# Optimization experiments

Measured on AMD Instinct MI355X. Metric: run time of the kernel, lower is better.

## Reference

```python
import jax, jax.numpy as jnp
import numpy as np

N, E, H, K = 50000, 300000, 128, 50
PI = float(np.pi)
EPS = 1e-5


def gaussian_expand(ea, k):
    # RBF expansion of each edge feature into k gaussians on [0, 1]
    centers = jnp.linspace(0.0, 1.0, k)            # (k,)
    width = 1.0 / k
    g = jnp.exp(-((ea[..., None] - centers) ** 2) / (2.0 * width * width))  # (E, 4, k)
    return g.reshape(ea.shape[0], -1)              # (E, 4k)


def bn_train(z, g, b):
    # BatchNorm1d in training mode: biased batch stats
    m = jnp.mean(z, axis=0)
    v = jnp.mean(z * z, axis=0) - m * m
    return (z - m) * jax.lax.rsqrt(v + EPS) * g + b


def lrelu(z):
    return jnp.where(z >= 0, z, 0.01 * z)


def setup_inputs() -> dict:
    key = jax.random.key(0)
    ks = jax.random.split(key, 16)
    s = 0.02
    d = {
        "x": jax.random.normal(ks[0], (N, H), jnp.float32),
        "edge_attr": jax.random.uniform(ks[1], (E, 4), jnp.float32),
        "edge_index": jax.random.randint(ks[2], (2, E), 0, N, jnp.int32),
        # f_b: Linear(4K -> H)
        "Wb": jax.random.normal(ks[3], (4 * K, H), jnp.float32) * s,
        "bb": jnp.zeros((H,), jnp.float32),
        # f_e: Linear(3H->H) + LReLU + BN + Linear(H->H) + LReLU + BN + Linear(H->H)
        "We1": jax.random.normal(ks[4], (3 * H, H), jnp.float32) * s,
        "be1": jnp.zeros((H,), jnp.float32),
        "ge1": jnp.ones((H,), jnp.float32),
        "bte1": jnp.zeros((H,), jnp.float32),
        "We2": jax.random.normal(ks[5], (H, H), jnp.float32) * s,
        "be2": jnp.zeros((H,), jnp.float32),
        "ge2": jnp.ones((H,), jnp.float32),
        "bte2": jnp.zeros((H,), jnp.float32),
        "We3": jax.random.normal(ks[6], (H, H), jnp.float32) * s,
        "be3": jnp.zeros((H,), jnp.float32),
        # f_d: Linear(H->H)
        "Wd": jax.random.normal(ks[7], (H, H), jnp.float32) * s,
        "bd": jnp.zeros((H,), jnp.float32),
        # v parameter (1, H)
        "v": jnp.ones((1, H), jnp.float32),
        # f_n: Linear(H->H) + LReLU + BN + Linear(H->H)
        "Wn1": jax.random.normal(ks[8], (H, H), jnp.float32) * s,
        "bn1": jnp.zeros((H,), jnp.float32),
        "gn": jnp.ones((H,), jnp.float32),
        "btn": jnp.zeros((H,), jnp.float32),
        "Wn2": jax.random.normal(ks[9], (H, H), jnp.float32) * s,
        "bn2": jnp.zeros((H,), jnp.float32),
    }
    return d


def reference(x, edge_attr, edge_index, Wb, bb, We1, be1, ge1, bte1, We2, be2,
              ge2, bte2, We3, be3, Wd, bd, v, Wn1, bn1, gn, btn, Wn2, bn2):
    src, dst = edge_index[0], edge_index[1]
    gt = gaussian_expand(edge_attr, K) @ Wb + bb            # (E, H)
    coeff = jnp.cos(PI / 2 * edge_attr[:, 3])[:, None]      # (E, 1)
    h = jnp.concatenate([x[src], gt, x[dst]], axis=1)       # (E, 3H)
    h = bn_train(lrelu(h @ We1 + be1), ge1, bte1)
    h = bn_train(lrelu(h @ We2 + be2), ge2, bte2)
    cond_filter = coeff * (h @ We3 + be3)                   # (E, H)
    m_st = cond_filter * (x[src] @ Wd + bd)                 # (E, H)
    m_t = v * (x @ Wd + bd)                                 # (N, H)
    incoming = jax.ops.segment_sum(m_st, dst, num_segments=N)  # scatter_add + zero pad
    z = m_t + incoming
    out = bn_train(lrelu(z @ Wn1 + bn1), gn, btn) @ Wn2 + bn2 + x
    return out
```

## Files before the change

kernel.cpp:

```cpp
#include <hip/hip_runtime.h>

typedef __attribute__((ext_vector_type(8))) short bf16x8;
typedef __attribute__((ext_vector_type(4))) float f32x4;
typedef __attribute__((ext_vector_type(4))) unsigned uint32x4;

#define DEVFN __device__ __forceinline__

DEVFN short f2bf(float f) {
    union { float f; unsigned u; } v; v.f = f;
    unsigned r = (v.u + 0x7FFFu + ((v.u >> 16) & 1u)) >> 16;
    return (short)(unsigned short)r;
}
DEVFN float bf2f(short h) {
    union { unsigned u; float f; } v; v.u = ((unsigned)(unsigned short)h) << 16;
    return v.f;
}
DEVFN unsigned pkbf(float a, float b) {
    unsigned r;
    asm("v_cvt_pk_bf16_f32 %0, %1, %2" : "=v"(r) : "v"(a), "v"(b));
    return r;
}

#define GLD_LDS16(gp, lp)                                                     \
    __builtin_amdgcn_global_load_lds(                                         \
        (const __attribute__((address_space(1))) unsigned*)(gp),              \
        (__attribute__((address_space(3))) unsigned*)(lp), 16, 0, 0)

struct __align__(16) ERec { int src; int dst; float cf; int pad; float4 ea; };



__global__ __launch_bounds__(128) void build_w1p_k(
    const float* __restrict__ Wb, const float* __restrict__ We1,
    const float* __restrict__ bb, const float* __restrict__ be1,
    float* __restrict__ W1p, float* __restrict__ b1p)
{
    int j = threadIdx.x;
    const float* B = We1 + 128 * 128;
    int i = blockIdx.x;
    if (i < 200) {
        float a = 0.f;
        for (int m = 0; m < 128; m++) a += Wb[i * 128 + m] * B[m * 128 + j];
        W1p[i * 128 + j] = a;
    } else {
        float a = be1[j];
        for (int m = 0; m < 128; m++) a += bb[m] * B[m * 128 + j];
        b1p[j] = a;
    }
}

__global__ __launch_bounds__(128) void build_tab_k(
    const float* __restrict__ W1p, const float* __restrict__ b1p,
    unsigned* __restrict__ tabP)
{
    int i = blockIdx.x;
    int c = blockIdx.y;
    int j = threadIdx.x;
    float t0 = (float)i * (1.0f / 1024.0f);
    float t1 = (float)(i + 1) * (1.0f / 1024.0f);
    float base = (c == 0) ? b1p[j] : 0.f;
    float a0 = base, a1 = base;
    int kc = (int)(t0 * 49.f + 0.5f);
    for (int dk = -6; dk <= 7; dk++) {
        int k = kc + dk;
        if (k >= 0 && k < 50) {
            float w = W1p[(c * 50 + k) * 128 + j];
            float d0 = t0 - (float)k * (1.f / 49.f);
            float d1 = t1 - (float)k * (1.f / 49.f);
            a0 += expf(-1250.f * d0 * d0) * w;
            a1 += expf(-1250.f * d1 * d1) * w;
        }
    }
    float v0 = bf2f(f2bf(a0));
    float v1 = bf2f(f2bf(a1));
    unsigned lo = (unsigned)(unsigned short)f2bf(a0);
    unsigned hi = (unsigned)(unsigned short)f2bf(v1 - v0);
    tabP[((size_t)(c * 1024 + i)) * 128 + j] = lo | (hi << 16);
}

__global__ __launch_bounds__(256) void fold_plain_k(
    const float* __restrict__ W0, const float* __restrict__ W1,
    const float* __restrict__ W2, const float* __restrict__ W3,
    short* __restrict__ O0, short* __restrict__ O1,
    short* __restrict__ O2, short* __restrict__ O3)
{
    const float* W = (blockIdx.y == 0) ? W0 : (blockIdx.y == 1) ? W1 : (blockIdx.y == 2) ? W2 : W3;
    short* O = (blockIdx.y == 0) ? O0 : (blockIdx.y == 1) ? O1 : (blockIdx.y == 2) ? O2 : O3;
    int idx = blockIdx.x * 256 + threadIdx.x;
    int n = idx >> 8, ks = (idx >> 6) & 3, lane = idx & 63;
    int k8 = ks * 32 + (lane >> 4) * 8;
    int pcol = (lane & 15) * 8 + n;
    bf16x8 fv;
    #pragma unroll
    for (int i2 = 0; i2 < 8; i2++) fv[i2] = f2bf(W[(k8 + i2) * 128 + pcol]);
    *(bf16x8*)(O + (size_t)idx * 8) = fv;
}

__global__ __launch_bounds__(256) void fold_k(
    const float* __restrict__ W, const float* __restrict__ bias,
    const float* __restrict__ statsG, const float* __restrict__ gamma,
    const float* __restrict__ beta, float invNs,
    short* __restrict__ Bp, float* __restrict__ biasOut)
{
    __shared__ float sS[128], sT[128];
    int tid = threadIdx.x;
    if (tid < 128) {
        float sum = 0.f, sq = 0.f;
        for (int r = 0; r < 16; r++) {
            sum += statsG[r * 256 + tid];
            sq  += statsG[r * 256 + 128 + tid];
        }
        float m = sum * invNs;
        float var = sq * invNs - m * m;
        float rs = rsqrtf(var + 1e-5f);
        float s = rs * gamma[tid];
        float t = beta[tid] - m * s;
        sS[tid] = s; sT[tid] = t;
    }
    __syncthreads();
    if (blockIdx.x == 0 && tid < 128) {
        float b = bias[tid];
        for (int k = 0; k < 128; k++) b += sT[k] * W[k * 128 + tid];
        biasOut[tid] = b;
    }
    int idx = blockIdx.x * 256 + tid;
    int n = idx >> 8, ks = (idx >> 6) & 3, lane = idx & 63;
    int k8 = ks * 32 + (lane >> 4) * 8;
    int pcol = (lane & 15) * 8 + n;
    bf16x8 fv;
    #pragma unroll
    for (int i2 = 0; i2 < 8; i2++)
        fv[i2] = f2bf(sS[k8 + i2] * W[(k8 + i2) * 128 + pcol]);
    *(bf16x8*)(Bp + (size_t)idx * 8) = fv;
}


__global__ __launch_bounds__(256) void hist_k(
    const int* __restrict__ dstI, int* __restrict__ cnt, int E)
{
    int e = blockIdx.x * 256 + threadIdx.x;
    if (e < E) atomicAdd(&cnt[dstI[e]], 1);
}

__global__ __launch_bounds__(256) void scan1_k(
    const int* __restrict__ cnt, int Nn, int* __restrict__ posE, int* __restrict__ bsum)
{
    __shared__ int s[256];
    int t = threadIdx.x, g = blockIdx.x * 256 + t;
    int v = (g < Nn) ? cnt[g] : 0;
    s[t] = v;
    __syncthreads();
    for (int off = 1; off < 256; off <<= 1) {
        int u = (t >= off) ? s[t - off] : 0;
        __syncthreads();
        s[t] += u;
        __syncthreads();
    }
    if (g < Nn) posE[g] = s[t] - v;
    if (t == 255) bsum[blockIdx.x] = s[255];
}

__global__ __launch_bounds__(256) void scan2_k(int* __restrict__ bsum, int nb)
{
    __shared__ int s[256];
    int t = threadIdx.x;
    int v = (t < nb) ? bsum[t] : 0;
    s[t] = v;
    __syncthreads();
    for (int off = 1; off < 256; off <<= 1) {
        int u = (t >= off) ? s[t - off] : 0;
        __syncthreads();
        s[t] += u;
        __syncthreads();
    }
    if (t < nb) bsum[t] = s[t] - v;
}

__global__ __launch_bounds__(256) void fix_k(
    const int* __restrict__ posE, const int* __restrict__ bsum,
    int* __restrict__ pos2, int Nn)
{
    int id = blockIdx.x * 256 + threadIdx.x;
    if (id < Nn) pos2[id] = posE[id] + bsum[id >> 8];
}

__global__ __launch_bounds__(256) void scat_k(
    const int* __restrict__ srcI, const int* __restrict__ dstI,
    const float4* __restrict__ ea4, int* __restrict__ pos2,
    ERec* __restrict__ rec, int E)
{
    int e = blockIdx.x * 256 + threadIdx.x;
    if (e >= E) return;
    int d = dstI[e];
    int p = atomicAdd(&pos2[d], 1);
    float4 ev = ea4[e];
    ERec r;
    r.src = srcI[e]; r.dst = d;
    r.cf = cosf(1.57079632679f * ev.w); r.pad = 0;
    r.ea = ev;
    rec[p] = r;
}

__global__ __launch_bounds__(256, 4) void node_all_k(
    const float* __restrict__ x, int M,
    const short* __restrict__ bp3,
    const float* __restrict__ bd, const float* __restrict__ vv,
    short* __restrict__ xd, short* __restrict__ zaccb,
    short* __restrict__ xs1b, short* __restrict__ xt1b)
{
    int tid = threadIdx.x;
    int wave = tid >> 6, lane = tid & 63;
    int kgrp = lane >> 4, colbase = lane & 15;
    int chunk = blockIdx.x;
    int rowA = chunk * 64 + wave * 16 + colbase;
    bool rv = rowA < M;

    bf16x8 af[4];
    #pragma unroll
    for (int ks = 0; ks < 4; ks++) {
        bf16x8 v = (bf16x8){0,0,0,0,0,0,0,0};
        if (rv) {
            const float* ap = x + (size_t)rowA * 128 + ks * 32 + kgrp * 8;
            float4 f0 = ((const float4*)ap)[0];
            float4 f1 = ((const float4*)ap)[1];
            v[0] = f2bf(f0.x); v[1] = f2bf(f0.y); v[2] = f2bf(f0.z); v[3] = f2bf(f0.w);
            v[4] = f2bf(f1.x); v[5] = f2bf(f1.y); v[6] = f2bf(f1.z); v[7] = f2bf(f1.w);
        }
        af[ks] = v;
    }

    float bcol[8], vcol[8];
    *(float4*)&bcol[0] = *(const float4*)(bd + colbase * 8);
    *(float4*)&bcol[4] = *(const float4*)(bd + colbase * 8 + 4);
    *(float4*)&vcol[0] = *(const float4*)(vv + colbase * 8);
    *(float4*)&vcol[4] = *(const float4*)(vv + colbase * 8 + 4);

    int rbase = chunk * 64 + wave * 16 + kgrp * 4;

    for (int b = 0; b < 3; b++) {
        const short* Bb = bp3 + (size_t)b * 16384;
        f32x4 acc[8];
        #pragma unroll
        for (int n = 0; n < 8; n++) acc[n] = (f32x4){0.f, 0.f, 0.f, 0.f};
        #pragma unroll
        for (int ks = 0; ks < 4; ks++) {
            #pragma unroll
            for (int n = 0; n < 8; n++) {
                bf16x8 bf = *(const bf16x8*)(Bb + ((size_t)((n * 4 + ks) * 64 + lane)) * 8);
                acc[n] = __builtin_amdgcn_mfma_f32_16x16x32_bf16(af[ks], bf, acc[n], 0, 0, 0);
            }
        }
        if (b == 0) {
            #pragma unroll
            for (int r = 0; r < 4; r++) {
                int row = rbase + r;
                if (row < M) {
                    bf16x8 xo, zo;
                    #pragma unroll
                    for (int n = 0; n < 8; n++) {
                        float val = acc[n][r] + bcol[n];
                        xo[n] = f2bf(val);
                        zo[n] = f2bf(vcol[n] * val);
                    }
                    *(bf16x8*)(xd    + (size_t)row * 128 + colbase * 8) = xo;
                    *(bf16x8*)(zaccb + (size_t)row * 128 + colbase * 8) = zo;
                }
            }
        } else {
            short* outp = (b == 1) ? xs1b : xt1b;
            #pragma unroll
            for (int r = 0; r < 4; r++) {
                int row = rbase + r;
                if (row < M) {
                    bf16x8 o;
                    #pragma unroll
                    for (int n = 0; n < 8; n++) o[n] = f2bf(acc[n][r]);
                    *(bf16x8*)(outp + (size_t)row * 128 + colbase * 8) = o;
                }
            }
        }
    }
}


#define EZ_ISSUE(XS, XT, TA, TB, FV, qi) do {                                  \
    int e_ = (qi) * 4 + esub;                                                  \
    int ec_ = e_ < Etot ? e_ : Etot - 1;                                       \
    const ERec* rp_ = rec + ec_;                                               \
    int4 h_ = *(const int4*)rp_;                                               \
    float4 ea_ = *(const float4*)((const char*)rp_ + 16);                      \
    int s_ = h_.x;                                                             \
    int d_ = h_.y;                                                             \
    XS = *(const bf16x8*)(xs1b + (size_t)s_ * 128 + colg * 8);                 \
    XT = *(const bf16x8*)(xt1b + (size_t)d_ * 128 + colg * 8);                 \
    float tv_[4] = {ea_.x, ea_.y, ea_.z, ea_.w};                               \
    _Pragma("unroll")                                                          \
    for (int c_ = 0; c_ < 4; c_++) {                                           \
        float u_ = tv_[c_] * 1024.f;                                           \
        int i0_ = (int)u_;                                                     \
        i0_ = i0_ < 0 ? 0 : (i0_ > 1023 ? 1023 : i0_);                         \
        FV[c_] = u_ - (float)i0_;                                              \
        const uint32x4* tp_ = (const uint32x4*)(tabP +                         \
            ((size_t)(c_ * 1024 + i0_) * 128) + colg * 8);                     \
        TA[c_] = tp_[0];                                                       \
        TB[c_] = tp_[1];                                                       \
    }                                                                          \
} while (0)

#define EZ_CONSUME(XS, XT, TA, TB, FV, qi) do {                                \
    int e_ = (qi) * 4 + esub;                                                  \
    float p_[8];                                                               \
    _Pragma("unroll")                                                          \
    for (int j_ = 0; j_ < 8; j_++) p_[j_] = bf2f(XS[j_]) + bf2f(XT[j_]);       \
    _Pragma("unroll")                                                          \
    for (int c_ = 0; c_ < 4; c_++) {                                           \
        float f_ = FV[c_];                                                     \
        _Pragma("unroll")                                                      \
        for (int j_ = 0; j_ < 4; j_++) {                                       \
            unsigned ua_ = TA[c_][j_];                                         \
            p_[j_] = fmaf(f_, __uint_as_float(ua_ & 0xffff0000u),              \
                          p_[j_] + __uint_as_float(ua_ << 16));                \
            unsigned ub_ = TB[c_][j_];                                         \
            p_[j_ + 4] = fmaf(f_, __uint_as_float(ub_ & 0xffff0000u),          \
                              p_[j_ + 4] + __uint_as_float(ub_ << 16));        \
        }                                                                      \
    }                                                                          \
    bool valid_ = e_ < Etot;                                                   \
    _Pragma("unroll")                                                          \
    for (int j_ = 0; j_ < 8; j_++) {                                           \
        float z_ = p_[j_] >= 0.f ? p_[j_] : 0.01f * p_[j_];                    \
        p_[j_] = z_;                                                           \
        float m_ = valid_ ? z_ : 0.f;                                          \
        sacc[j_] += m_;                                                        \
        qacc[j_] = fmaf(m_, z_, qacc[j_]);                                     \
    }                                                                          \
    if (valid_) {                                                              \
        uint32x4 ov_ = {pkbf(p_[0], p_[1]), pkbf(p_[2], p_[3]),                \
                        pkbf(p_[4], p_[5]), pkbf(p_[6], p_[7])};               \
        *(uint32x4*)(z1 + (size_t)e_ * 128 + colg * 8) = ov_;                  \
    }                                                                          \
} while (0)

__global__ __launch_bounds__(256) void edge_z1_k(
    const short* __restrict__ xs1b, const short* __restrict__ xt1b,
    const unsigned* __restrict__ tabP,
    const ERec* __restrict__ rec,
    short* __restrict__ z1, float* __restrict__ stats, int Etot)
{
    int tid = threadIdx.x, wave = tid >> 6, lane = tid & 63;
    int colg = lane & 15, esub = lane >> 4;

    int gw = blockIdx.x * 4 + wave;
    int W = gridDim.x * 4;
    int nq = (Etot + 3) >> 2;
    int q0 = (int)(((long long)gw * nq) / W);
    int q1 = (int)(((long long)(gw + 1) * nq) / W);
    int nsteps = q1 - q0;

    float sacc[8], qacc[8];
    #pragma unroll
    for (int j = 0; j < 8; j++) { sacc[j] = 0.f; qacc[j] = 0.f; }

    bf16x8 xsA, xtA; uint32x4 taA[4], tbA[4]; float fvA[4];
    bf16x8 xsB, xtB; uint32x4 taB[4], tbB[4]; float fvB[4];
    bf16x8 xsC, xtC; uint32x4 taC[4], tbC[4]; float fvC[4];

    if (nsteps > 0) {
        EZ_ISSUE(xsA, xtA, taA, tbA, fvA, q0 + 0);
        EZ_ISSUE(xsB, xtB, taB, tbB, fvB, q0 + 1);
        int st = 0;
        for (; st + 3 <= nsteps; st += 3) {
            EZ_ISSUE(xsC, xtC, taC, tbC, fvC, q0 + st + 2);
            EZ_CONSUME(xsA, xtA, taA, tbA, fvA, q0 + st);
            EZ_ISSUE(xsA, xtA, taA, tbA, fvA, q0 + st + 3);
            EZ_CONSUME(xsB, xtB, taB, tbB, fvB, q0 + st + 1);
            EZ_ISSUE(xsB, xtB, taB, tbB, fvB, q0 + st + 4);
            EZ_CONSUME(xsC, xtC, taC, tbC, fvC, q0 + st + 2);
        }
        if (st < nsteps)
            EZ_CONSUME(xsA, xtA, taA, tbA, fvA, q0 + st);
        if (st + 1 < nsteps)
            EZ_CONSUME(xsB, xtB, taB, tbB, fvB, q0 + st + 1);
    }

    #pragma unroll
    for (int j = 0; j < 8; j++) {
        sacc[j] += __shfl_xor(sacc[j], 16);
        sacc[j] += __shfl_xor(sacc[j], 32);
        qacc[j] += __shfl_xor(qacc[j], 16);
        qacc[j] += __shfl_xor(qacc[j], 32);
    }

    __shared__ float lS[128], lQ[128];
    if (tid < 128) { lS[tid] = 0.f; lQ[tid] = 0.f; }
    __syncthreads();
    if (esub == 0) {
        #pragma unroll
        for (int j = 0; j < 8; j++) {
            atomicAdd(&lS[colg * 8 + j], sacc[j]);
            atomicAdd(&lQ[colg * 8 + j], qacc[j]);
        }
    }
    __syncthreads();
    if (tid < 128) {
        int rep = blockIdx.x & 15;
        atomicAdd(&stats[rep * 256 + tid], lS[tid]);
        atomicAdd(&stats[rep * 256 + 128 + tid], lQ[tid]);
    }
}

__global__ __launch_bounds__(256) void segred_k(
    const short* __restrict__ cond, const short* __restrict__ xd,
    const ERec* __restrict__ rec, const int* __restrict__ endPos,
    short* __restrict__ zaccb, int Nn)
{
    int tid = threadIdx.x, wave = tid >> 6, lane = tid & 63;
    int colg = lane & 7;
    int esub = lane >> 3;
    int d0 = blockIdx.x * 32 + wave * 8;

    for (int i = 0; i < 8; i++) {
        int d = d0 + i;
        if (d >= Nn) break;
        int s0 = (d == 0) ? 0 : endPos[d - 1];
        int s1 = endPos[d];
        if (s1 <= s0) continue;

        float acc[16];
        #pragma unroll
        for (int j = 0; j < 16; j++) acc[j] = 0.f;

        for (int t = s0 + esub; t < s1; t += 8) {
            const short* cp = cond + (size_t)t * 128 + colg * 16;
            bf16x8 c0 = *(const bf16x8*)cp;
            bf16x8 c1 = *(const bf16x8*)(cp + 8);
            int s = rec[t].src;
            const short* xp = xd + (size_t)s * 128 + colg * 16;
            bf16x8 x0 = *(const bf16x8*)xp;
            bf16x8 x1 = *(const bf16x8*)(xp + 8);
            #pragma unroll
            for (int j = 0; j < 8; j++) {
                acc[j]     += bf2f(c0[j]) * bf2f(x0[j]);
                acc[8 + j] += bf2f(c1[j]) * bf2f(x1[j]);
            }
        }

        #pragma unroll
        for (int j = 0; j < 16; j++) {
            acc[j] += __shfl_xor(acc[j], 8);
            acc[j] += __shfl_xor(acc[j], 16);
            acc[j] += __shfl_xor(acc[j], 32);
        }

        if (esub == 0) {
            short* zp = zaccb + (size_t)d * 128 + colg * 16;
            bf16x8 z0 = *(const bf16x8*)zp;
            bf16x8 z1 = *(const bf16x8*)(zp + 8);
            bf16x8 o0, o1;
            #pragma unroll
            for (int j = 0; j < 8; j++) {
                o0[j] = f2bf(bf2f(z0[j]) + acc[j]);
                o1[j] = f2bf(bf2f(z1[j]) + acc[8 + j]);
            }
            *(bf16x8*)zp = o0;
            *(bf16x8*)(zp + 8) = o1;
        }
    }
}

template<int EPI>
__global__ __launch_bounds__(256, 2) void pgemm_k(
    const short* __restrict__ A, int M,
    const short* __restrict__ Bp, const float* __restrict__ bias,
    void* __restrict__ out, float* __restrict__ stats,
    const ERec* __restrict__ rec, const float* __restrict__ xres)
{
    __shared__ __align__(16) short ldsB[16384];
    __shared__ float lS[128], lQ[128];
    int tid = threadIdx.x;
    int wave = tid >> 6, lane = tid & 63;
    int kgrp = lane >> 4, colbase = lane & 15;

    #pragma unroll
    for (int i = 0; i < 8; i++) {
        int off = (i * 256 + wave * 64 + lane) * 8;
        GLD_LDS16(Bp + off, ldsB + off);
    }

    int nch = (M + 63) >> 6;
    int cbeg = (int)(((long long)blockIdx.x * nch) / gridDim.x);
    int cend = (int)(((long long)(blockIdx.x + 1) * nch) / gridDim.x);

    bf16x8 afc[4];
    {
        int rowA = cbeg * 64 + wave * 16 + colbase;
        bool rv = (cbeg < cend) && (rowA < M);
        #pragma unroll
        for (int ks = 0; ks < 4; ks++)
            afc[ks] = rv ? *(const bf16x8*)(A + (size_t)rowA * 128 + ks * 32 + kgrp * 8)
                         : (bf16x8){0,0,0,0,0,0,0,0};
    }

    float bcol[8];
    *(float4*)&bcol[0] = *(const float4*)(bias + colbase * 8);
    *(float4*)&bcol[4] = *(const float4*)(bias + colbase * 8 + 4);

    float sreg[8], qreg[8];
    if (EPI == 2) {
        #pragma unroll
        for (int n = 0; n < 8; n++) { sreg[n] = 0.f; qreg[n] = 0.f; }
        if (tid < 128) { lS[tid] = 0.f; lQ[tid] = 0.f; }
    }

    __syncthreads();

    for (int c = cbeg; c < cend; c++) {
        int cn = c + 1;
        bf16x8 afn[4];
        {
            int rowA = cn * 64 + wave * 16 + colbase;
            bool rv = (cn < cend) && (rowA < M);
            #pragma unroll
            for (int ks = 0; ks < 4; ks++)
                afn[ks] = rv ? *(const bf16x8*)(A + (size_t)rowA * 128 + ks * 32 + kgrp * 8)
                             : (bf16x8){0,0,0,0,0,0,0,0};
        }

        int rbase = c * 64 + wave * 16 + kgrp * 4;

        float mcf[4];
        if (EPI == 3) {
            #pragma unroll
            for (int r = 0; r < 4; r++) {
                int row = rbase + r;
                mcf[r] = (row < M) ? rec[row].cf : 0.f;
            }
        }

        f32x4 acc[8];
        #pragma unroll
        for (int n = 0; n < 8; n++) acc[n] = (f32x4){0.f, 0.f, 0.f, 0.f};
        #pragma unroll
        for (int ks = 0; ks < 4; ks++) {
            #pragma unroll
            for (int n = 0; n < 8; n++) {
                bf16x8 bf = *(const bf16x8*)(ldsB + ((size_t)((n * 4 + ks) * 64 + lane)) * 8);
                acc[n] = __builtin_amdgcn_mfma_f32_16x16x32_bf16(afc[ks], bf, acc[n], 0, 0, 0);
            }
        }

        if (EPI == 2) {
            short* outh = (short*)out;
            #pragma unroll
            for (int r = 0; r < 4; r++) {
                int row = rbase + r;
                float zz[8];
                #pragma unroll
                for (int n = 0; n < 8; n++) {
                    float z = acc[n][r] + bcol[n];
                    z = z >= 0.f ? z : 0.01f * z;
                    if (row >= M) z = 0.f;
                    sreg[n] += z; qreg[n] += z * z;
                    zz[n] = z;
                }
                if (row < M) {
                    uint32x4 ov = {pkbf(zz[0], zz[1]), pkbf(zz[2], zz[3]),
                                   pkbf(zz[4], zz[5]), pkbf(zz[6], zz[7])};
                    *(uint32x4*)(outh + (size_t)row * 128 + colbase * 8) = ov;
                }
            }
        } else if (EPI == 3) {
            short* outh = (short*)out;
            #pragma unroll
            for (int r = 0; r < 4; r++) {
                int row = rbase + r;
                if (row < M) {
                    float zz[8];
                    #pragma unroll
                    for (int n = 0; n < 8; n++)
                        zz[n] = mcf[r] * (acc[n][r] + bcol[n]);
                    uint32x4 ov = {pkbf(zz[0], zz[1]), pkbf(zz[2], zz[3]),
                                   pkbf(zz[4], zz[5]), pkbf(zz[6], zz[7])};
                    *(uint32x4*)(outh + (size_t)row * 128 + colbase * 8) = ov;
                }
            }
        } else if (EPI == 4) {
            float* outf = (float*)out;
            #pragma unroll
            for (int r = 0; r < 4; r++) {
                int row = rbase + r;
                if (row < M) {
                    const float4* xr = (const float4*)(xres + (size_t)row * 128 + colbase * 8);
                    float4 x0 = xr[0], x1 = xr[1];
                    float4 o0, o1;
                    o0.x = acc[0][r] + bcol[0] + x0.x;
                    o0.y = acc[1][r] + bcol[1] + x0.y;
                    o0.z = acc[2][r] + bcol[2] + x0.z;
                    o0.w = acc[3][r] + bcol[3] + x0.w;
                    o1.x = acc[4][r] + bcol[4] + x1.x;
                    o1.y = acc[5][r] + bcol[5] + x1.y;
                    o1.z = acc[6][r] + bcol[6] + x1.z;
                    o1.w = acc[7][r] + bcol[7] + x1.w;
                    float4* op = (float4*)(outf + (size_t)row * 128 + colbase * 8);
                    op[0] = o0; op[1] = o1;
                }
            }
        }

        #pragma unroll
        for (int ks = 0; ks < 4; ks++) afc[ks] = afn[ks];
    }

    if (EPI == 2) {
        __syncthreads();
        #pragma unroll
        for (int n = 0; n < 8; n++) {
            atomicAdd(&lS[colbase * 8 + n], sreg[n]);
            atomicAdd(&lQ[colbase * 8 + n], qreg[n]);
        }
        __syncthreads();
        if (tid < 128) {
            int rep = blockIdx.x & 15;
            atomicAdd(&stats[rep * 256 + tid], lS[tid]);
            atomicAdd(&stats[rep * 256 + 128 + tid], lQ[tid]);
        }
    }
}

extern "C" void kernel_launch(void* const* d_in, const int* in_sizes, int n_in,
                              void* d_out, int out_size, void* d_ws, size_t ws_size,
                              hipStream_t stream)
{
    const float* x    = (const float*)d_in[0];
    const float* ea   = (const float*)d_in[1];
    const int*   eidx = (const int*)d_in[2];
    const float* Wb   = (const float*)d_in[3];
    const float* bb   = (const float*)d_in[4];
    const float* We1  = (const float*)d_in[5];
    const float* be1  = (const float*)d_in[6];
    const float* ge1  = (const float*)d_in[7];
    const float* bte1 = (const float*)d_in[8];
    const float* We2  = (const float*)d_in[9];
    const float* be2  = (const float*)d_in[10];
    const float* ge2  = (const float*)d_in[11];
    const float* bte2 = (const float*)d_in[12];
    const float* We3  = (const float*)d_in[13];
    const float* be3  = (const float*)d_in[14];
    const float* Wd   = (const float*)d_in[15];
    const float* bd   = (const float*)d_in[16];
    const float* vv   = (const float*)d_in[17];
    const float* Wn1  = (const float*)d_in[18];
    const float* bn1  = (const float*)d_in[19];
    const float* gn   = (const float*)d_in[20];
    const float* btn  = (const float*)d_in[21];
    const float* Wn2  = (const float*)d_in[22];
    const float* bn2  = (const float*)d_in[23];

    const int NN = in_sizes[0] / 128;
    const int EE = in_sizes[1] / 4;

    char* ws = (char*)d_ws;
    size_t oEZ   = 0;
    size_t oXD   = oEZ   + (size_t)EE * 256;
    size_t oXS   = oXD   + (size_t)NN * 256;
    size_t oXT   = oXS   + (size_t)NN * 256;
    size_t oZACC = oXT   + (size_t)NN * 256;
    size_t oZN   = oZACC + (size_t)NN * 256;
    size_t oTAB  = oZN   + (size_t)NN * 256;
    size_t oW1P  = oTAB  + (size_t)4 * 1024 * 512;
    size_t oB1P  = oW1P  + (size_t)200 * 512;
    size_t oBP   = oB1P  + 512;
    size_t oBIAS = oBP   + (size_t)7 * 32768;
    size_t oST   = oBIAS + (size_t)7 * 512;
    size_t oCNT  = oST   + 49152;
    size_t oPOS  = oCNT  + 201728;
    size_t oBSUM = oPOS  + 201728;
    size_t oPOS2 = oBSUM + 1024;
    size_t oREC  = (oPOS2 + 201728 + 31) & ~(size_t)31;

    short* eZ    = (short*)(ws + oEZ);
    short* xd    = (short*)(ws + oXD);
    short* xs1b  = (short*)(ws + oXS);
    short* xt1b  = (short*)(ws + oXT);
    short* zaccb = (short*)(ws + oZACC);
    short* zn    = (short*)(ws + oZN);
    unsigned* tabP = (unsigned*)(ws + oTAB);
    float* W1p   = (float*)(ws + oW1P);
    float* b1p   = (float*)(ws + oB1P);
    short* bp    = (short*)(ws + oBP);
    short* BpW2  = bp + 3 * 16384;
    short* BpW3  = bp + 4 * 16384;
    short* BpN1  = bp + 5 * 16384;
    short* BpN2  = bp + 6 * 16384;
    float* bo    = (float*)(ws + oBIAS);
    float* b2p   = bo + 0 * 128;
    float* b3p   = bo + 1 * 128;
    float* b2np  = bo + 2 * 128;
    float* st1   = (float*)(ws + oST);
    float* st2   = st1 + 4096;
    float* stN   = st1 + 8192;
    int*   cnt   = (int*)(ws + oCNT);
    int*   posE  = (int*)(ws + oPOS);
    int*   bsum  = (int*)(ws + oBSUM);
    int*   pos2  = (int*)(ws + oPOS2);
    ERec*  rec   = (ERec*)(ws + oREC);

    hipMemsetAsync(ws + oST, 0, 49152 + 201728, stream);

    build_w1p_k<<<201, 128, 0, stream>>>(Wb, We1, bb, be1, W1p, b1p);
    build_tab_k<<<dim3(1024, 4), 128, 0, stream>>>(W1p, b1p, tabP);
    fold_plain_k<<<dim3(8, 4), 256, 0, stream>>>(
        Wd, We1, We1 + 256 * 128, Wn1, bp, bp + 16384, bp + 2 * 16384, BpN1);

    int nchN = (NN + 63) / 64;
    int nchE = (EE + 63) / 64;
    int nbN = (NN + 255) / 256;
    int nbE = (EE + 255) / 256;
    int nbSeg = (NN + 31) / 32;

    int gridEz = 1024;
    int gridE = nchE < 1024 ? nchE : 1024;
    int gridN = nchN < 512 ? nchN : 512;

    node_all_k<<<nchN, 256, 0, stream>>>(x, NN, bp, bd, vv, xd, zaccb, xs1b, xt1b);

    hist_k<<<nbE, 256, 0, stream>>>(eidx + EE, cnt, EE);
    scan1_k<<<nbN, 256, 0, stream>>>(cnt, NN, posE, bsum);
    scan2_k<<<1, 256, 0, stream>>>(bsum, nbN);
    fix_k<<<nbN, 256, 0, stream>>>(posE, bsum, pos2, NN);
    scat_k<<<nbE, 256, 0, stream>>>(eidx, eidx + EE, (const float4*)ea, pos2,
                                    rec, EE);

    edge_z1_k<<<gridEz, 256, 0, stream>>>(xs1b, xt1b, tabP, rec, eZ, st1, EE);

    fold_k<<<8, 256, 0, stream>>>(We2, be2, st1, ge1, bte1, 1.f / (float)EE, BpW2, b2p);
    pgemm_k<2><<<gridE, 256, 0, stream>>>(eZ, EE, BpW2, b2p, eZ, st2,
        nullptr, nullptr);

    fold_k<<<8, 256, 0, stream>>>(We3, be3, st2, ge2, bte2, 1.f / (float)EE, BpW3, b3p);
    pgemm_k<3><<<gridE, 256, 0, stream>>>(eZ, EE, BpW3, b3p, eZ, nullptr,
        rec, nullptr);

    segred_k<<<nbSeg, 256, 0, stream>>>(eZ, xd, rec, pos2, zaccb, NN);

    pgemm_k<2><<<gridN, 256, 0, stream>>>(zaccb, NN, BpN1, bn1, zn, stN,
        nullptr, nullptr);

    fold_k<<<8, 256, 0, stream>>>(Wn2, bn2, stN, gn, btn, 1.f / (float)NN, BpN2, b2np);
    pgemm_k<4><<<gridN, 256, 0, stream>>>(zn, NN, BpN2, b2np, d_out, nullptr,
        nullptr, x);
}
```

Baseline: 400.8 us.

## Use finer nearest-neighbor bf16 Gaussian table and deepen A-fragment prefetch in pgemm

```diff
diff --git a/kernel.cpp b/kernel.cpp
--- a/kernel.cpp
+++ b/kernel.cpp
@@ -51,31 +51,23 @@
 
 __global__ __launch_bounds__(128) void build_tab_k(
     const float* __restrict__ W1p, const float* __restrict__ b1p,
-    unsigned* __restrict__ tabP)
+    short* __restrict__ tabN)
 {
     int i = blockIdx.x;
     int c = blockIdx.y;
     int j = threadIdx.x;
-    float t0 = (float)i * (1.0f / 1024.0f);
-    float t1 = (float)(i + 1) * (1.0f / 1024.0f);
-    float base = (c == 0) ? b1p[j] : 0.f;
-    float a0 = base, a1 = base;
-    int kc = (int)(t0 * 49.f + 0.5f);
-    for (int dk = -6; dk <= 7; dk++) {
+    float t = ((float)i + 0.5f) * (1.0f / 4096.0f);
+    float acc = (c == 0) ? b1p[j] : 0.f;
+    int kc = (int)(t * 49.f + 0.5f);
+    for (int dk = -6; dk <= 6; dk++) {
         int k = kc + dk;
         if (k >= 0 && k < 50) {
-            float w = W1p[(c * 50 + k) * 128 + j];
-            float d0 = t0 - (float)k * (1.f / 49.f);
-            float d1 = t1 - (float)k * (1.f / 49.f);
-            a0 += expf(-1250.f * d0 * d0) * w;
-            a1 += expf(-1250.f * d1 * d1) * w;
-        }
-    }
-    float v0 = bf2f(f2bf(a0));
-    float v1 = bf2f(f2bf(a1));
-    unsigned lo = (unsigned)(unsigned short)f2bf(a0);
-    unsigned hi = (unsigned)(unsigned short)f2bf(v1 - v0);
-    tabP[((size_t)(c * 1024 + i)) * 128 + j] = lo | (hi << 16);
+            float d = t - (float)k * (1.f / 49.f);
+            float g = expf(-1250.f * d * d);
+            acc += g * W1p[(c * 50 + k) * 128 + j];
+        }
+    }
+    tabN[((size_t)(c * 4096 + i)) * 128 + j] = f2bf(acc);
 }
 
 __global__ __launch_bounds__(256) void fold_plain_k(
@@ -283,47 +275,33 @@
 }
 
 
-#define EZ_ISSUE(XS, XT, TA, TB, FV, qi) do {                                  \
+#define EZ_ISSUE(XS, XT, TT, qi) do {                                          \
     int e_ = (qi) * 4 + esub;                                                  \
     int ec_ = e_ < Etot ? e_ : Etot - 1;                                       \
     const ERec* rp_ = rec + ec_;                                               \
     int4 h_ = *(const int4*)rp_;                                               \
     float4 ea_ = *(const float4*)((const char*)rp_ + 16);                      \
-    int s_ = h_.x;                                                             \
-    int d_ = h_.y;                                                             \
-    XS = *(const bf16x8*)(xs1b + (size_t)s_ * 128 + colg * 8);                 \
-    XT = *(const bf16x8*)(xt1b + (size_t)d_ * 128 + colg * 8);                 \
+    XS = *(const bf16x8*)(xs1b + (size_t)h_.x * 128 + colg * 8);               \
+    XT = *(const bf16x8*)(xt1b + (size_t)h_.y * 128 + colg * 8);               \
     float tv_[4] = {ea_.x, ea_.y, ea_.z, ea_.w};                               \
     _Pragma("unroll")                                                          \
     for (int c_ = 0; c_ < 4; c_++) {                                           \
-        float u_ = tv_[c_] * 1024.f;                                           \
-        int i0_ = (int)u_;                                                     \
-        i0_ = i0_ < 0 ? 0 : (i0_ > 1023 ? 1023 : i0_);                         \
-        FV[c_] = u_ - (float)i0_;                                              \
-        const uint32x4* tp_ = (const uint32x4*)(tabP +                         \
-            ((size_t)(c_ * 1024 + i0_) * 128) + colg * 8);                     \
-        TA[c_] = tp_[0];                                                       \
-        TB[c_] = tp_[1];                                                       \
+        int i0_ = (int)(tv_[c_] * 4096.f);                                     \
+        i0_ = i0_ < 0 ? 0 : (i0_ > 4095 ? 4095 : i0_);                         \
+        TT[c_] = *(const bf16x8*)(tabN +                                       \
+            ((size_t)(c_ * 4096 + i0_) * 128) + colg * 8);                     \
     }                                                                          \
 } while (0)
 
-#define EZ_CONSUME(XS, XT, TA, TB, FV, qi) do {                                \
+#define EZ_CONSUME(XS, XT, TT, qi) do {                                        \
     int e_ = (qi) * 4 + esub;                                                  \
     float p_[8];                                                               \
     _Pragma("unroll")                                                          \
     for (int j_ = 0; j_ < 8; j_++) p_[j_] = bf2f(XS[j_]) + bf2f(XT[j_]);       \
     _Pragma("unroll")                                                          \
     for (int c_ = 0; c_ < 4; c_++) {                                           \
-        float f_ = FV[c_];                                                     \
         _Pragma("unroll")                                                      \
-        for (int j_ = 0; j_ < 4; j_++) {                                       \
-            unsigned ua_ = TA[c_][j_];                                         \
-            p_[j_] = fmaf(f_, __uint_as_float(ua_ & 0xffff0000u),              \
-                          p_[j_] + __uint_as_float(ua_ << 16));                \
-            unsigned ub_ = TB[c_][j_];                                         \
-            p_[j_ + 4] = fmaf(f_, __uint_as_float(ub_ & 0xffff0000u),          \
-                              p_[j_ + 4] + __uint_as_float(ub_ << 16));        \
-        }                                                                      \
+        for (int j_ = 0; j_ < 8; j_++) p_[j_] += bf2f(TT[c_][j_]);             \
     }                                                                          \
     bool valid_ = e_ < Etot;                                                   \
     _Pragma("unroll")                                                          \
@@ -343,7 +321,7 @@
 
 __global__ __launch_bounds__(256) void edge_z1_k(
     const short* __restrict__ xs1b, const short* __restrict__ xt1b,
-    const unsigned* __restrict__ tabP,
+    const short* __restrict__ tabN,
     const ERec* __restrict__ rec,
     short* __restrict__ z1, float* __restrict__ stats, int Etot)
 {
@@ -361,26 +339,26 @@
     #pragma unroll
     for (int j = 0; j < 8; j++) { sacc[j] = 0.f; qacc[j] = 0.f; }
 
-    bf16x8 xsA, xtA; uint32x4 taA[4], tbA[4]; float fvA[4];
-    bf16x8 xsB, xtB; uint32x4 taB[4], tbB[4]; float fvB[4];
-    bf16x8 xsC, xtC; uint32x4 taC[4], tbC[4]; float fvC[4];
+    bf16x8 xsA, xtA, ttA[4];
+    bf16x8 xsB, xtB, ttB[4];
+    bf16x8 xsC, xtC, ttC[4];
 
     if (nsteps > 0) {
-        EZ_ISSUE(xsA, xtA, taA, tbA, fvA, q0 + 0);
-        EZ_ISSUE(xsB, xtB, taB, tbB, fvB, q0 + 1);
+        EZ_ISSUE(xsA, xtA, ttA, q0 + 0);
+        EZ_ISSUE(xsB, xtB, ttB, q0 + 1);
         int st = 0;
         for (; st + 3 <= nsteps; st += 3) {
-            EZ_ISSUE(xsC, xtC, taC, tbC, fvC, q0 + st + 2);
-            EZ_CONSUME(xsA, xtA, taA, tbA, fvA, q0 + st);
-            EZ_ISSUE(xsA, xtA, taA, tbA, fvA, q0 + st + 3);
-            EZ_CONSUME(xsB, xtB, taB, tbB, fvB, q0 + st + 1);
-            EZ_ISSUE(xsB, xtB, taB, tbB, fvB, q0 + st + 4);
-            EZ_CONSUME(xsC, xtC, taC, tbC, fvC, q0 + st + 2);
+            EZ_ISSUE(xsC, xtC, ttC, q0 + st + 2);
+            EZ_CONSUME(xsA, xtA, ttA, q0 + st);
+            EZ_ISSUE(xsA, xtA, ttA, q0 + st + 3);
+            EZ_CONSUME(xsB, xtB, ttB, q0 + st + 1);
+            EZ_ISSUE(xsB, xtB, ttB, q0 + st + 4);
+            EZ_CONSUME(xsC, xtC, ttC, q0 + st + 2);
         }
         if (st < nsteps)
-            EZ_CONSUME(xsA, xtA, taA, tbA, fvA, q0 + st);
+            EZ_CONSUME(xsA, xtA, ttA, q0 + st);
         if (st + 1 < nsteps)
-            EZ_CONSUME(xsB, xtB, taB, tbB, fvB, q0 + st + 1);
+            EZ_CONSUME(xsB, xtB, ttB, q0 + st + 1);
     }
 
     #pragma unroll
@@ -491,13 +469,22 @@
     int cbeg = (int)(((long long)blockIdx.x * nch) / gridDim.x);
     int cend = (int)(((long long)(blockIdx.x + 1) * nch) / gridDim.x);
 
-    bf16x8 afc[4];
+    bf16x8 afA[4], afB[4];
     {
         int rowA = cbeg * 64 + wave * 16 + colbase;
         bool rv = (cbeg < cend) && (rowA < M);
         #pragma unroll
         for (int ks = 0; ks < 4; ks++)
-            afc[ks] = rv ? *(const bf16x8*)(A + (size_t)rowA * 128 + ks * 32 + kgrp * 8)
+            afA[ks] = rv ? *(const bf16x8*)(A + (size_t)rowA * 128 + ks * 32 + kgrp * 8)
+                         : (bf16x8){0,0,0,0,0,0,0,0};
+    }
+    {
+        int c1 = cbeg + 1;
+        int rowA = c1 * 64 + wave * 16 + colbase;
+        bool rv = (c1 < cend) && (rowA < M);
+        #pragma unroll
+        for (int ks = 0; ks < 4; ks++)
+            afB[ks] = rv ? *(const bf16x8*)(A + (size_t)rowA * 128 + ks * 32 + kgrp * 8)
                          : (bf16x8){0,0,0,0,0,0,0,0};
     }
 
@@ -515,14 +502,14 @@
     __syncthreads();
 
     for (int c = cbeg; c < cend; c++) {
-        int cn = c + 1;
-        bf16x8 afn[4];
+        int cn = c + 2;
+        bf16x8 afN[4];
         {
             int rowA = cn * 64 + wave * 16 + colbase;
             bool rv = (cn < cend) && (rowA < M);
             #pragma unroll
             for (int ks = 0; ks < 4; ks++)
-                afn[ks] = rv ? *(const bf16x8*)(A + (size_t)rowA * 128 + ks * 32 + kgrp * 8)
+                afN[ks] = rv ? *(const bf16x8*)(A + (size_t)rowA * 128 + ks * 32 + kgrp * 8)
                              : (bf16x8){0,0,0,0,0,0,0,0};
         }
 
@@ -545,7 +532,7 @@
             #pragma unroll
             for (int n = 0; n < 8; n++) {
                 bf16x8 bf = *(const bf16x8*)(ldsB + ((size_t)((n * 4 + ks) * 64 + lane)) * 8);
-                acc[n] = __builtin_amdgcn_mfma_f32_16x16x32_bf16(afc[ks], bf, acc[n], 0, 0, 0);
+                acc[n] = __builtin_amdgcn_mfma_f32_16x16x32_bf16(afA[ks], bf, acc[n], 0, 0, 0);
             }
         }
 
@@ -608,7 +595,7 @@
         }
 
         #pragma unroll
-        for (int ks = 0; ks < 4; ks++) afc[ks] = afn[ks];
+        for (int ks = 0; ks < 4; ks++) { afA[ks] = afB[ks]; afB[ks] = afN[ks]; }
     }
 
     if (EPI == 2) {
@@ -667,7 +654,7 @@
     size_t oZACC = oXT   + (size_t)NN * 256;
     size_t oZN   = oZACC + (size_t)NN * 256;
     size_t oTAB  = oZN   + (size_t)NN * 256;
-    size_t oW1P  = oTAB  + (size_t)4 * 1024 * 512;
+    size_t oW1P  = oTAB  + (size_t)4 * 4096 * 256;
     size_t oB1P  = oW1P  + (size_t)200 * 512;
     size_t oBP   = oB1P  + 512;
     size_t oBIAS = oBP   + (size_t)7 * 32768;
@@ -684,7 +671,7 @@
     short* xt1b  = (short*)(ws + oXT);
     short* zaccb = (short*)(ws + oZACC);
     short* zn    = (short*)(ws + oZN);
-    unsigned* tabP = (unsigned*)(ws + oTAB);
+    short* tabN  = (short*)(ws + oTAB);
     float* W1p   = (float*)(ws + oW1P);
     float* b1p   = (float*)(ws + oB1P);
     short* bp    = (short*)(ws + oBP);
@@ -708,7 +695,7 @@
     hipMemsetAsync(ws + oST, 0, 49152 + 201728, stream);
 
     build_w1p_k<<<201, 128, 0, stream>>>(Wb, We1, bb, be1, W1p, b1p);
-    build_tab_k<<<dim3(1024, 4), 128, 0, stream>>>(W1p, b1p, tabP);
+    build_tab_k<<<dim3(4096, 4), 128, 0, stream>>>(W1p, b1p, tabN);
     fold_plain_k<<<dim3(8, 4), 256, 0, stream>>>(
         Wd, We1, We1 + 256 * 128, Wn1, bp, bp + 16384, bp + 2 * 16384, BpN1);
 
@@ -731,7 +718,7 @@
     scat_k<<<nbE, 256, 0, stream>>>(eidx, eidx + EE, (const float4*)ea, pos2,
                                     rec, EE);
 
-    edge_z1_k<<<gridEz, 256, 0, stream>>>(xs1b, xt1b, tabP, rec, eZ, st1, EE);
+    edge_z1_k<<<gridEz, 256, 0, stream>>>(xs1b, xt1b, tabN, rec, eZ, st1, EE);
 
     fold_k<<<8, 256, 0, stream>>>(We2, be2, st1, ge1, bte1, 1.f / (float)EE, BpW2, b2p);
     pgemm_k<2><<<gridE, 256, 0, stream>>>(eZ, EE, BpW2, b2p, eZ, st2,
```

Measured after the change: 415.2 us. 3.6% more time.
